# Optimization experiments

Measured on AMD Instinct MI355X. Metric: run time of the kernel, lower is better.

## Reference

```python
import jax, jax.numpy as jnp
import numpy as np

DIM = 128
HEADS = 4
DH = 32
TOPK_RATIO = 0.25
MIN_TOPK = 32
Q_KEEP_RATIO = 0.75
MIN_Q_KEEP = 64
NEG = -1e30


def _layernorm(x, g, b, eps=1e-5):
    mu = x.mean(-1, keepdims=True)
    var = ((x - mu) ** 2).mean(-1, keepdims=True)
    return (x - mu) * jax.lax.rsqrt(var + eps) * g + b


def _topk_scatter_mask(x, k):
    # boolean mask with True at the top-k entries along the last axis (torch scatter_ semantics)
    shp = x.shape
    x2 = x.reshape(-1, shp[-1])
    _, idx = jax.lax.top_k(x2, k)
    rows = jnp.arange(x2.shape[0])[:, None]
    m = jnp.zeros(x2.shape, dtype=bool).at[rows, idx].set(True)
    return m.reshape(shp)


def setup_inputs() -> dict:
    key = jax.random.key(0)
    ks = jax.random.split(key, 24)
    b, n = 1, 6
    x_, y_ = 6, 6
    qw1, qw2 = 16, 16
    kw1, kw2 = 8, 8
    s = 0.02
    inp = {
        'q': jax.random.normal(ks[0], (b, n, x_, y_, qw1, qw2, DIM), jnp.float32),
        'k': jax.random.normal(ks[1], (b, n, x_, y_, kw1, kw2, DIM), jnp.float32),
        'v': jax.random.normal(ks[2], (b, n, x_, y_, kw1, kw2, DIM), jnp.float32),
        'skip': jax.random.normal(ks[3], (b, x_, y_, qw1, qw2, DIM), jnp.float32),
        'logit_bias': jax.random.normal(ks[4], (b, n, 1, 1), jnp.float32),
        'g_q': jnp.ones((DIM,), jnp.float32), 'b_q': jnp.zeros((DIM,), jnp.float32),
        'g_k': jnp.ones((DIM,), jnp.float32), 'b_k': jnp.zeros((DIM,), jnp.float32),
        'g_v': jnp.ones((DIM,), jnp.float32), 'b_v': jnp.zeros((DIM,), jnp.float32),
        'Wq': jax.random.normal(ks[5], (DIM, HEADS * DH), jnp.float32) * s,
        'bq': jnp.zeros((HEADS * DH,), jnp.float32),
        'Wk': jax.random.normal(ks[6], (DIM, HEADS * DH), jnp.float32) * s,
        'bk': jnp.zeros((HEADS * DH,), jnp.float32),
        'Wv': jax.random.normal(ks[7], (DIM, HEADS * DH), jnp.float32) * s,
        'bv': jnp.zeros((HEADS * DH,), jnp.float32),
        'Wp': jax.random.normal(ks[8], (HEADS * DH, DIM), jnp.float32) * s,
        'bp': jnp.zeros((DIM,), jnp.float32),
    }
    return inp


def reference(q, k, v, skip, logit_bias, g_q, b_q, g_k, b_k, g_v, b_v,
              Wq, bq, Wk, bk, Wv, bv, Wp, bp):
    b, n, xh, yw, qw1, qw2, d = q.shape
    _, _, _, _, kw1, kw2, _ = k.shape
    L = xh * yw
    Qn = n * qw1 * qw2
    Kn = n * kw1 * kw2
    H, Dh = HEADS, DH
    scale = Dh ** -0.5

    def win(t, w1, w2, N):
        # b n x y w1 w2 d -> b (x y) (n w1 w2) d
        t = jnp.transpose(t, (0, 2, 3, 1, 4, 5, 6))
        return t.reshape(b, L, N, d)

    qt = win(q, qw1, qw2, Qn)
    kt = win(k, kw1, kw2, Kn)
    vt = win(v, kw1, kw2, Kn)

    qt = _layernorm(qt, g_q, b_q) @ Wq + bq
    kt = _layernorm(kt, g_k, b_k) @ Wk + bk
    vt = _layernorm(vt, g_v, b_v) @ Wv + bv

    def heads(t, N):
        # b l t (h d) -> (b h) l t d
        t = t.reshape(b, L, N, H, Dh)
        t = jnp.transpose(t, (0, 3, 1, 2, 4))
        return t.reshape(b * H, L, N, Dh)

    qh = heads(qt, Qn)
    kh = heads(kt, Kn)
    vh = heads(vt, Kn)

    # dynamic query pruning: keep top-keep_q queries by squared-norm saliency
    keep_q = min(max(max(int(Qn * Q_KEEP_RATIO), MIN_Q_KEEP), 1), Qn)
    sal = jnp.sum(qh * qh, axis=-1)                 # (bh, L, Qn)
    qmask = _topk_scatter_mask(sal, keep_q)
    qh = qh * qmask[..., None]

    logits = jnp.einsum('blqd,blkd->blqk', qh * scale, kh)  # (bh, L, Qn, Kn)

    # OAPE additive logit bias: mean over cameras, tiled (bh index i -> batch i % b)
    lb = logit_bias.mean(axis=1).reshape(b)          # (b,)
    lb_bh = jnp.tile(lb, H)                          # (b*h,) ordering i % b (torch .repeat)
    logits = logits + lb_bh[:, None, None, None]

    topk = max(int(Kn * TOPK_RATIO), MIN_TOPK)
    kmask = _topk_scatter_mask(logits, topk)
    logits = jnp.where(kmask, logits, NEG)
    att = jax.nn.softmax(logits, axis=-1)

    a = jnp.einsum('blqk,blkd->blqd', att, vh)       # (bh, L, Qn, Dh)
    # (b h) l (n w1 w2) d -> b n x y w1 w2 (h d)
    a = a.reshape(b, H, L, n, qw1, qw2, Dh)
    a = jnp.transpose(a, (0, 3, 2, 4, 5, 1, 6)).reshape(b, n, xh, yw, qw1, qw2, H * Dh)

    z = a @ Wp + bp
    z = z.mean(axis=1)                               # mean over cameras
    z = z + skip
    return z
```

## Files before the change

kernel.cpp:

```cpp
#include <hip/hip_runtime.h>
#include <hip/hip_bf16.h>


#define LWIN  36
#define QN    1536
#define KN    384
#define QHS_E 1769472
#define KHS_E 442368
#define KEEPQ 1152

#define SQ_SCALE (0.17677669529663687f * 1.4426950408889634f)

typedef unsigned short ushort_t;
typedef __attribute__((ext_vector_type(8))) short bf16x8;
typedef __attribute__((ext_vector_type(4))) float f32x4;

__device__ __forceinline__ float us2f(unsigned short u) { return __uint_as_float(((unsigned)u) << 16); }
__device__ __forceinline__ unsigned short f2us(float f) { return (unsigned short)(__float_as_uint(f) >> 16); }

__device__ __forceinline__ float fast_exp2(float x) {
#if __has_builtin(__builtin_amdgcn_exp2f)
    return __builtin_amdgcn_exp2f(x);
#else
    return exp2f(x);
#endif
}

__device__ __forceinline__ int wfrag_pos(int k, int n) {
    return ((n >> 4) * 4 + (k >> 5)) * 512 + ((k >> 3) & 3) * 128 + (n & 15) * 8 + (k & 7);
}

__global__ __launch_bounds__(256)
void prep_w_kernel(const float* __restrict__ W0, const float* __restrict__ W1,
                   const float* __restrict__ W2, const float* __restrict__ W3,
                   ushort_t* __restrict__ outw)
{
    const float* W = (blockIdx.x == 0) ? W0 : (blockIdx.x == 1) ? W1
                   : (blockIdx.x == 2) ? W2 : W3;
    const float scl = (blockIdx.x == 0) ? SQ_SCALE : 1.0f;
    __shared__ __align__(16) ushort_t L[16384];
    const int tid = threadIdx.x;
    for (int i = 0; i < 64; ++i) {
        int idx = tid + i * 256;
        int k = idx >> 7, n = idx & 127;
        L[wfrag_pos(k, n)] = f2us(W[idx] * scl);
    }
    __syncthreads();
    uint4* dst = (uint4*)(outw + (size_t)blockIdx.x * 16384);
    const uint4* src = (const uint4*)L;
    for (int i = 0; i < 8; ++i) dst[tid + i * 256] = src[tid + i * 256];
}

__global__ __launch_bounds__(256, 4)
void gemm_proj_kernel(const float* __restrict__ xq, const float* __restrict__ xk,
                      const float* __restrict__ xv,
                      const float* __restrict__ g_q, const float* __restrict__ b_q,
                      const float* __restrict__ g_k, const float* __restrict__ b_k,
                      const float* __restrict__ g_v, const float* __restrict__ b_v,
                      const ushort_t* __restrict__ Wfb,
                      const float* __restrict__ bq, const float* __restrict__ bk,
                      const float* __restrict__ bv,
                      ushort_t* __restrict__ Qh, ushort_t* __restrict__ Kh,
                      ushort_t* __restrict__ Vt, float* __restrict__ sal)
{
    __shared__ __align__(16) ushort_t SB[8704];
    __shared__ __align__(16) float redA[256], redB[256];
    __shared__ float2 mr[64];

    const int b = blockIdx.x;
    const float *xin, *gvec, *bvec, *bias;
    const ushort_t* wf;
    ushort_t* outp;
    float* salp = nullptr;
    int lw2, lw12, ntok, hs_e, mode, t0;
    float bscale = 1.0f;
    if (b < 864) {
        xin = xq; gvec = g_q; bvec = b_q; wf = Wfb; bias = bq; outp = Qh;
        salp = sal; lw2 = 4; lw12 = 8; ntok = QN; hs_e = QHS_E; mode = 0;
        t0 = b * 64; bscale = SQ_SCALE;
    } else if (b < 1080) {
        xin = xk; gvec = g_k; bvec = b_k; wf = Wfb + 16384; bias = bk; outp = Kh;
        lw2 = 3; lw12 = 6; ntok = KN; hs_e = KHS_E; mode = 0; t0 = (b - 864) * 64;
    } else {
        xin = xv; gvec = g_v; bvec = b_v; wf = Wfb + 32768; bias = bv; outp = Vt;
        lw2 = 3; lw12 = 6; ntok = KN; hs_e = 0; mode = 1; t0 = (b - 1080) * 64;
    }

    const int tid = threadIdx.x;

    const int tok = tid >> 2, seg = tid & 3;
    float f[32];
    {
        int t = t0 + tok;
        int l = t / ntok, qn = t - l * ntok;
        int n = qn >> lw12, rr = qn & ((1 << lw12) - 1);
        int a1 = rr >> lw2, a2 = rr & ((1 << lw2) - 1);
        int x = l / 6, y = l - 6 * x;
        size_t off = (size_t)(((((n * 6 + x) * 6 + y) << lw12) + (a1 << lw2) + a2)) * 128;
        const float4* xp = (const float4*)(xin + off) + seg * 8;
        float s = 0.f, s2 = 0.f;
#pragma unroll
        for (int j = 0; j < 8; ++j) {
            float4 v = xp[j];
            f[4 * j + 0] = v.x; f[4 * j + 1] = v.y; f[4 * j + 2] = v.z; f[4 * j + 3] = v.w;
            s += v.x + v.y + v.z + v.w;
            s2 += v.x * v.x + v.y * v.y + v.z * v.z + v.w * v.w;
        }
        redA[tid] = s; redB[tid] = s2;
    }
    __syncthreads();
    if (tid < 64) {
        float4 sa = *(float4*)&redA[tid * 4];
        float4 sb = *(float4*)&redB[tid * 4];
        float s = sa.x + sa.y + sa.z + sa.w;
        float s2 = sb.x + sb.y + sb.z + sb.w;
        float mu = s * (1.0f / 128.0f);
        float var = s2 * (1.0f / 128.0f) - mu * mu;
        mr[tid] = make_float2(mu, rsqrtf(var + 1e-5f));
    }
    __syncthreads();
    {
        float2 m = mr[tok];
#pragma unroll
        for (int qd = 0; qd < 4; ++qd) {
            const float4 g0 = *(const float4*)&gvec[seg * 32 + qd * 8];
            const float4 g1 = *(const float4*)&gvec[seg * 32 + qd * 8 + 4];
            const float4 b0 = *(const float4*)&bvec[seg * 32 + qd * 8];
            const float4 b1 = *(const float4*)&bvec[seg * 32 + qd * 8 + 4];
            float v[8];
            v[0] = (f[qd*8+0] - m.x) * m.y * g0.x + b0.x;
            v[1] = (f[qd*8+1] - m.x) * m.y * g0.y + b0.y;
            v[2] = (f[qd*8+2] - m.x) * m.y * g0.z + b0.z;
            v[3] = (f[qd*8+3] - m.x) * m.y * g0.w + b0.w;
            v[4] = (f[qd*8+4] - m.x) * m.y * g1.x + b1.x;
            v[5] = (f[qd*8+5] - m.x) * m.y * g1.y + b1.y;
            v[6] = (f[qd*8+6] - m.x) * m.y * g1.z + b1.z;
            v[7] = (f[qd*8+7] - m.x) * m.y * g1.w + b1.w;
            uint4 pk;
            pk.x = (unsigned)f2us(v[0]) | ((unsigned)f2us(v[1]) << 16);
            pk.y = (unsigned)f2us(v[2]) | ((unsigned)f2us(v[3]) << 16);
            pk.z = (unsigned)f2us(v[4]) | ((unsigned)f2us(v[5]) << 16);
            pk.w = (unsigned)f2us(v[6]) | ((unsigned)f2us(v[7]) << 16);
            *(uint4*)&SB[((tok >> 4) * 4 + seg) * 512 + qd * 128 + (tok & 15) * 8] = pk;
        }
    }
    __syncthreads();

    const int wv = tid >> 6, lane = tid & 63;
    const int col = lane & 15, quad = lane >> 4;
    f32x4 acc[8];
#pragma unroll
    for (int nt = 0; nt < 8; ++nt) acc[nt] = (f32x4){0.f, 0.f, 0.f, 0.f};
#pragma unroll
    for (int ks = 0; ks < 4; ++ks) {
        bf16x8 a = *(const bf16x8*)&SB[((wv * 4 + ks) * 64 + lane) * 8];
#pragma unroll
        for (int nt = 0; nt < 8; ++nt) {
            bf16x8 bfr = *(const bf16x8*)&wf[((nt * 4 + ks) * 64 + lane) * 8];
            acc[nt] = __builtin_amdgcn_mfma_f32_16x16x32_bf16(a, bfr, acc[nt], 0, 0, 0);
        }
    }
#pragma unroll
    for (int nt = 0; nt < 8; ++nt) {
        float bvv = bias[nt * 16 + col] * bscale;
#pragma unroll
        for (int r = 0; r < 4; ++r) acc[nt][r] += bvv;
    }

    if (salp) {
        float p[4][4];
#pragma unroll
        for (int h = 0; h < 4; ++h)
#pragma unroll
            for (int r = 0; r < 4; ++r)
                p[h][r] = acc[2*h][r] * acc[2*h][r] + acc[2*h+1][r] * acc[2*h+1][r];
#pragma unroll
        for (int sh = 1; sh < 16; sh <<= 1)
#pragma unroll
            for (int h = 0; h < 4; ++h)
#pragma unroll
                for (int r = 0; r < 4; ++r) p[h][r] += __shfl_xor(p[h][r], sh);
        if (col < 4) {
#pragma unroll
            for (int r = 0; r < 4; ++r)
                salp[(size_t)col * (LWIN * ntok) + (t0 + wv * 16 + quad * 4 + r)] = p[col][r];
        }
    }

    __syncthreads();
    if (mode == 0) {
#pragma unroll
        for (int nt = 0; nt < 8; ++nt)
#pragma unroll
            for (int r = 0; r < 4; ++r)
                SB[(nt >> 1) * 2048 + (wv * 16 + quad * 4 + r) * 32 + (nt & 1) * 16 + col] =
                    f2us(acc[nt][r]);
        __syncthreads();
#pragma unroll
        for (int i = 0; i < 4; ++i) {
            int idx16 = tid + i * 256;
            int hh = idx16 >> 8, rem = idx16 & 255;
            *(uint4*)(outp + (size_t)hh * hs_e + (size_t)t0 * 32 + rem * 8) =
                *(const uint4*)&SB[hh * 2048 + rem * 8];
        }
    } else {
#pragma unroll
        for (int nt = 0; nt < 8; ++nt)
#pragma unroll
            for (int r = 0; r < 4; ++r)
                SB[(nt >> 1) * 2176 + ((nt & 1) * 16 + col) * 68 + wv * 16 + quad * 4 + r] =
                    f2us(acc[nt][r]);
        __syncthreads();
        const int l = t0 / KN, kb = t0 - l * KN;
#pragma unroll
        for (int i = 0; i < 2; ++i) {
            int idx16 = tid + i * 256;
            int hh = idx16 >> 7, rem = idx16 & 127;
            int dh = rem >> 2, c = rem & 3;
            *(uint4*)(outp + ((size_t)(hh * LWIN + l) * 32 + dh) * KN + kb + c * 8) =
                *(const uint4*)&SB[hh * 2176 + dh * 68 + c * 8];
        }
    }
}

__global__ __launch_bounds__(64)
void prune_kernel(const float* __restrict__ sal, const ushort_t* __restrict__ Vt,
                  ushort_t* __restrict__ Qh, ushort_t* __restrict__ kidx)
{
    __shared__ __align__(16) ushort_t VmS[32];
    const int lane = threadIdx.x;
    const int h = blockIdx.x / LWIN, l = blockIdx.x % LWIN;

    if (lane < 32) {
        const ushort_t* vrow = Vt + ((size_t)(h * LWIN + l) * 32 + lane) * KN;
        float s = 0.f;
#pragma unroll
        for (int j = 0; j < 96; ++j) s += us2f(vrow[j]);
        VmS[lane] = f2us(s * (1.0f / 96.0f));
    }

    const float* srow = sal + (size_t)h * (LWIN * QN) + (size_t)l * QN;
    unsigned u[24];
#pragma unroll
    for (int i = 0; i < 24; ++i)
        u[i] = __float_as_uint(srow[lane * 24 + i]);

    unsigned lo = 0u, hi = 0x80000000u;
#pragma unroll 1
    while (hi - lo > 1u) {
        unsigned mid = lo + ((hi - lo) >> 1);
        int c = 0;
#pragma unroll
        for (int i = 0; i < 24; ++i) c += (u[i] >= mid);
#pragma unroll
        for (int sh = 32; sh > 0; sh >>= 1) c += __shfl_xor(c, sh);
        if (c >= KEEPQ) lo = mid; else hi = mid;
    }
    const unsigned T = lo;

    int c_gt = 0, eqc = 0;
    int eqpos[24];
#pragma unroll
    for (int i = 0; i < 24; ++i) {
        c_gt += (u[i] > T);
        eqpos[i] = eqc;
        eqc += (u[i] == T);
    }
    int cg = c_gt;
#pragma unroll
    for (int sh = 32; sh > 0; sh >>= 1) cg += __shfl_xor(cg, sh);
    int scanE = eqc;
#pragma unroll
    for (int sh = 1; sh < 64; sh <<= 1) {
        int t = __shfl_up(scanE, sh);
        if (lane >= sh) scanE += t;
    }
    const int preE = scanE - eqc;
    const int need = KEEPQ - cg;

    bool keep[24];
    int kc = 0;
#pragma unroll
    for (int i = 0; i < 24; ++i) {
        keep[i] = (u[i] > T) || ((u[i] == T) && (preE + eqpos[i] < need));
        kc += keep[i];
    }
    int scanK = kc;
#pragma unroll
    for (int sh = 1; sh < 64; sh <<= 1) {
        int t = __shfl_up(scanK, sh);
        if (lane >= sh) scanK += t;
    }
    int posK = scanK - kc;

    __syncthreads();
    const uint4 vm0 = *(const uint4*)&VmS[0];
    const uint4 vm1 = *(const uint4*)&VmS[8];
    const uint4 vm2 = *(const uint4*)&VmS[16];
    const uint4 vm3 = *(const uint4*)&VmS[24];

    ushort_t* kout  = kidx + (size_t)(h * LWIN + l) * KEEPQ;
    ushort_t* qbase = Qh + (size_t)h * QHS_E + (size_t)l * QN * 32;
#pragma unroll 1
    for (int i = 0; i < 24; ++i) {
        if (keep[i]) {
            kout[posK++] = (ushort_t)(lane * 24 + i);
        } else {
            uint4* p = (uint4*)(qbase + (size_t)(lane * 24 + i) * 32);
            p[0] = vm0; p[1] = vm1; p[2] = vm2; p[3] = vm3;
        }
    }
}

__global__ __launch_bounds__(256, 3)
void attn_kernel(ushort_t* __restrict__ Qh, const ushort_t* __restrict__ Kh,
                 const ushort_t* __restrict__ Vt, const ushort_t* __restrict__ kidx)
{
    __shared__ __align__(16) ushort_t Ks[KN * 36];
    __shared__ __align__(16) ushort_t Vs[32 * 390];

    const int tid = threadIdx.x;
    const int qt = blockIdx.x, l = blockIdx.y, h = blockIdx.z;

    const ushort_t* kg = Kh + (size_t)h * KHS_E + (size_t)l * (KN * 32);
#pragma unroll
    for (int i = 0; i < 12; ++i) {
        int idx = tid + i * 256;
        int key = idx >> 3, c = idx & 7;
        *(uint2*)&Ks[key * 36 + c * 4] = *(const uint2*)&kg[idx * 4];
    }
    const ushort_t* vg = Vt + (size_t)(h * LWIN + l) * (32 * KN);
#pragma unroll
    for (int i = 0; i < 12; ++i) {
        int idx = tid + i * 256;
        int dh = idx / 96, c = idx - dh * 96;
        *(uint2*)&Vs[dh * 390 + c * 4] = *(const uint2*)&vg[idx * 4];
    }

    const int lane = tid & 63, wv = tid >> 6;
    const int col = lane & 15, quad = lane >> 4;

    const ushort_t* kr = kidx + (size_t)(h * LWIN + l) * KEEPQ + qt * 64 + wv * 16;
    const int rowA = kr[col];
    const ushort_t* qhl = Qh + (size_t)h * QHS_E + (size_t)l * QN * 32;
    const bf16x8 aq = *(const bf16x8*)(qhl + (size_t)rowA * 32 + quad * 8);
    __syncthreads();

    f32x4 s[24];
#pragma unroll
    for (int t = 0; t < 24; ++t) s[t] = (f32x4){0.f, 0.f, 0.f, 0.f};
#pragma unroll
    for (int t = 0; t < 24; ++t) {
        bf16x8 bk = *(const bf16x8*)&Ks[(16 * t + col) * 36 + quad * 8];
        s[t] = __builtin_amdgcn_mfma_f32_16x16x32_bf16(aq, bk, s[t], 0, 0, 0);
    }
    __syncthreads();

    float vmax[4], vmin[4];
#pragma unroll
    for (int r = 0; r < 4; ++r) { vmax[r] = s[0][r]; vmin[r] = s[0][r]; }
#pragma unroll
    for (int t = 1; t < 24; ++t)
#pragma unroll
        for (int r = 0; r < 4; ++r) {
            vmax[r] = fmaxf(vmax[r], s[t][r]);
            vmin[r] = fminf(vmin[r], s[t][r]);
        }
#pragma unroll
    for (int sh = 1; sh < 16; sh <<= 1)
#pragma unroll
        for (int r = 0; r < 4; ++r) {
            vmax[r] = fmaxf(vmax[r], __shfl_xor(vmax[r], sh));
            vmin[r] = fminf(vmin[r], __shfl_xor(vmin[r], sh));
        }

    float lo[4], hi[4];
#pragma unroll
    for (int r = 0; r < 4; ++r) { lo[r] = vmin[r] - 1.0f; hi[r] = vmax[r]; }
    for (int it = 0; it < 10; ++it) {
        float mid[4]; int cnt[4];
#pragma unroll
        for (int r = 0; r < 4; ++r) { mid[r] = 0.5f * (lo[r] + hi[r]); cnt[r] = 0; }
#pragma unroll
        for (int t = 0; t < 24; ++t)
#pragma unroll
            for (int r = 0; r < 4; ++r) cnt[r] += (s[t][r] > mid[r]);
#pragma unroll
        for (int sh = 1; sh < 16; sh <<= 1)
#pragma unroll
            for (int r = 0; r < 4; ++r) cnt[r] += __shfl_xor(cnt[r], sh);
#pragma unroll
        for (int r = 0; r < 4; ++r) {
            if (cnt[r] >= 96) lo[r] = mid[r]; else hi[r] = mid[r];
        }
    }

    float sum[4];
#pragma unroll
    for (int r = 0; r < 4; ++r) sum[r] = 0.f;
#pragma unroll
    for (int t = 0; t < 24; ++t)
#pragma unroll
        for (int r = 0; r < 4; ++r) {
            float e = (s[t][r] > lo[r]) ? fast_exp2(s[t][r] - vmax[r]) : 0.f;
            s[t][r] = e; sum[r] += e;
        }
#pragma unroll
    for (int sh = 1; sh < 16; sh <<= 1)
#pragma unroll
        for (int r = 0; r < 4; ++r) sum[r] += __shfl_xor(sum[r], sh);
    float inv[4];
#pragma unroll
    for (int r = 0; r < 4; ++r) inv[r] = 1.0f / sum[r];

    f32x4 o0 = (f32x4){0.f, 0.f, 0.f, 0.f};
    f32x4 o1 = (f32x4){0.f, 0.f, 0.f, 0.f};
    ushort_t* pb = Ks + wv * 1088;
#pragma unroll
    for (int ch = 0; ch < 6; ++ch) {
#pragma unroll
        for (int tl = 0; tl < 4; ++tl) {
            int t = 4 * ch + tl;
#pragma unroll
            for (int r = 0; r < 4; ++r)
                pb[(quad * 4 + r) * 68 + 16 * tl + col] = f2us(s[t][r]);
        }
#pragma unroll
        for (int ks = 0; ks < 2; ++ks) {
            bf16x8 ap  = *(const bf16x8*)&pb[col * 68 + ks * 32 + quad * 8];
            bf16x8 bv0 = *(const bf16x8*)&Vs[col * 390 + ch * 64 + ks * 32 + quad * 8];
            bf16x8 bv1 = *(const bf16x8*)&Vs[(16 + col) * 390 + ch * 64 + ks * 32 + quad * 8];
            o0 = __builtin_amdgcn_mfma_f32_16x16x32_bf16(ap, bv0, o0, 0, 0, 0);
            o1 = __builtin_amdgcn_mfma_f32_16x16x32_bf16(ap, bv1, o1, 0, 0, 0);
        }
    }

#pragma unroll
    for (int r = 0; r < 4; ++r) {
        ushort_t* oq = (ushort_t*)qhl + (size_t)kr[quad * 4 + r] * 32;
        oq[col]      = f2us(o0[r] * inv[r]);
        oq[16 + col] = f2us(o1[r] * inv[r]);
    }
}

__global__ __launch_bounds__(256, 4)
void gemm_out_kernel(const ushort_t* __restrict__ aS,
                     const ushort_t* __restrict__ Wfrag,
                     const float* __restrict__ bp,
                     const float* __restrict__ skip,
                     float* __restrict__ outp)
{
    __shared__ __align__(16) ushort_t SB[8192];

    const int tid = threadIdx.x;
    const int t0 = blockIdx.x * 64;

    const int tok = tid >> 2, h = tid & 3;
    {
        int t = t0 + tok;
        int l = t >> 8, qq = t & 255;
        float f[32];
#pragma unroll
        for (int e = 0; e < 32; ++e) f[e] = 0.f;
#pragma unroll
        for (int n = 0; n < 6; ++n) {
            const ushort_t* p = aS + (size_t)h * QHS_E + ((size_t)l * QN + n * 256 + qq) * 32;
#pragma unroll
            for (int c = 0; c < 4; ++c) {
                ushort4 va = *(const ushort4*)(p + c * 8);
                ushort4 vb = *(const ushort4*)(p + c * 8 + 4);
                f[c*8+0] += us2f(va.x); f[c*8+1] += us2f(va.y);
                f[c*8+2] += us2f(va.z); f[c*8+3] += us2f(va.w);
                f[c*8+4] += us2f(vb.x); f[c*8+5] += us2f(vb.y);
                f[c*8+6] += us2f(vb.z); f[c*8+7] += us2f(vb.w);
            }
        }
#pragma unroll
        for (int qd = 0; qd < 4; ++qd) {
            uint4 pk;
            pk.x = (unsigned)f2us(f[qd*8+0] * (1.f/6.f)) | ((unsigned)f2us(f[qd*8+1] * (1.f/6.f)) << 16);
            pk.y = (unsigned)f2us(f[qd*8+2] * (1.f/6.f)) | ((unsigned)f2us(f[qd*8+3] * (1.f/6.f)) << 16);
            pk.z = (unsigned)f2us(f[qd*8+4] * (1.f/6.f)) | ((unsigned)f2us(f[qd*8+5] * (1.f/6.f)) << 16);
            pk.w = (unsigned)f2us(f[qd*8+6] * (1.f/6.f)) | ((unsigned)f2us(f[qd*8+7] * (1.f/6.f)) << 16);
            *(uint4*)&SB[((tok >> 4) * 4 + h) * 512 + qd * 128 + (tok & 15) * 8] = pk;
        }
    }
    __syncthreads();

    const int wv = tid >> 6, lane = tid & 63;
    const int col = lane & 15, quad = lane >> 4;
    f32x4 acc[8];
#pragma unroll
    for (int nt = 0; nt < 8; ++nt) acc[nt] = (f32x4){0.f, 0.f, 0.f, 0.f};
#pragma unroll
    for (int ks = 0; ks < 4; ++ks) {
        bf16x8 a = *(const bf16x8*)&SB[((wv * 4 + ks) * 64 + lane) * 8];
#pragma unroll
        for (int nt = 0; nt < 8; ++nt) {
            bf16x8 bfr = *(const bf16x8*)&Wfrag[((nt * 4 + ks) * 64 + lane) * 8];
            acc[nt] = __builtin_amdgcn_mfma_f32_16x16x32_bf16(a, bfr, acc[nt], 0, 0, 0);
        }
    }
#pragma unroll
    for (int nt = 0; nt < 8; ++nt) {
        float bv = bp[nt * 16 + col];
#pragma unroll
        for (int r = 0; r < 4; ++r) {
            int trow = t0 + wv * 16 + quad * 4 + r;
            size_t gi = (size_t)trow * 128 + nt * 16 + col;
            outp[gi] = acc[nt][r] + bv + skip[gi];
        }
    }
}

extern "C" void kernel_launch(void* const* d_in, const int* in_sizes, int n_in,
                              void* d_out, int out_size, void* d_ws, size_t ws_size,
                              hipStream_t stream)
{
    (void)in_sizes; (void)n_in; (void)out_size; (void)ws_size;
    const float* q    = (const float*)d_in[0];
    const float* k    = (const float*)d_in[1];
    const float* v    = (const float*)d_in[2];
    const float* skip = (const float*)d_in[3];
    const float* g_q = (const float*)d_in[5];
    const float* b_q = (const float*)d_in[6];
    const float* g_k = (const float*)d_in[7];
    const float* b_k = (const float*)d_in[8];
    const float* g_v = (const float*)d_in[9];
    const float* b_v = (const float*)d_in[10];
    const float* Wq  = (const float*)d_in[11];
    const float* bq  = (const float*)d_in[12];
    const float* Wk  = (const float*)d_in[13];
    const float* bk  = (const float*)d_in[14];
    const float* Wv  = (const float*)d_in[15];
    const float* bv  = (const float*)d_in[16];
    const float* Wp  = (const float*)d_in[17];
    const float* bp  = (const float*)d_in[18];

    ushort_t* Qh = (ushort_t*)d_ws;
    ushort_t* Kh = Qh + (size_t)4 * QHS_E;
    ushort_t* Vt = Kh + (size_t)4 * KHS_E;
    float*   sal = (float*)(Vt + (size_t)4 * KHS_E);
    ushort_t* Wf = (ushort_t*)(sal + (size_t)4 * LWIN * QN);
    ushort_t* kidx = Wf + (size_t)4 * 16384;

    prep_w_kernel<<<4, 256, 0, stream>>>(Wq, Wk, Wv, Wp, Wf);
    gemm_proj_kernel<<<1296, 256, 0, stream>>>(q, k, v, g_q, b_q, g_k, b_k, g_v, b_v,
                                               Wf, bq, bk, bv, Qh, Kh, Vt, sal);
    prune_kernel<<<144, 64, 0, stream>>>(sal, Vt, Qh, kidx);
    attn_kernel<<<dim3(18, LWIN, 4), 256, 0, stream>>>(Qh, Kh, Vt, kidx);
    gemm_out_kernel<<<144, 256, 0, stream>>>(Qh, Wf + 3 * 16384, bp, skip, (float*)d_out);
}
```

Before: 269.0 us.

## Split small kernels across more blocks and narrow top-k bisection range

```diff
diff --git a/kernel.cpp b/kernel.cpp
--- a/kernel.cpp
+++ b/kernel.cpp
@@ -35,20 +35,21 @@
                    const float* __restrict__ W2, const float* __restrict__ W3,
                    ushort_t* __restrict__ outw)
 {
-    const float* W = (blockIdx.x == 0) ? W0 : (blockIdx.x == 1) ? W1
-                   : (blockIdx.x == 2) ? W2 : W3;
-    const float scl = (blockIdx.x == 0) ? SQ_SCALE : 1.0f;
-    __shared__ __align__(16) ushort_t L[16384];
+    const int m = blockIdx.x >> 1, half = blockIdx.x & 1;
+    const float* W = (m == 0) ? W0 : (m == 1) ? W1 : (m == 2) ? W2 : W3;
+    const float scl = (m == 0) ? SQ_SCALE : 1.0f;
+    __shared__ __align__(16) ushort_t L[8192];
     const int tid = threadIdx.x;
-    for (int i = 0; i < 64; ++i) {
+    const int nbase = half * 64;
+    for (int i = 0; i < 32; ++i) {
         int idx = tid + i * 256;
-        int k = idx >> 7, n = idx & 127;
-        L[wfrag_pos(k, n)] = f2us(W[idx] * scl);
-    }
-    __syncthreads();
-    uint4* dst = (uint4*)(outw + (size_t)blockIdx.x * 16384);
+        int k = idx >> 6, n0 = idx & 63;
+        L[wfrag_pos(k, nbase + n0) - half * 8192] = f2us(W[k * 128 + nbase + n0] * scl);
+    }
+    __syncthreads();
+    uint4* dst = (uint4*)(outw + (size_t)m * 16384 + half * 8192);
     const uint4* src = (const uint4*)L;
-    for (int i = 0; i < 8; ++i) dst[tid + i * 256] = src[tid + i * 256];
+    for (int i = 0; i < 4; ++i) dst[tid + i * 256] = src[tid + i * 256];
 }
 
 __global__ __launch_bounds__(256, 4)
@@ -231,12 +232,18 @@
     const int lane = threadIdx.x;
     const int h = blockIdx.x / LWIN, l = blockIdx.x % LWIN;
 
-    if (lane < 32) {
-        const ushort_t* vrow = Vt + ((size_t)(h * LWIN + l) * 32 + lane) * KN;
+    {
+        const int dh = lane >> 1, hf = lane & 1;
+        const ushort_t* vrow = Vt + ((size_t)(h * LWIN + l) * 32 + dh) * KN + hf * 48;
         float s = 0.f;
 #pragma unroll
-        for (int j = 0; j < 96; ++j) s += us2f(vrow[j]);
-        VmS[lane] = f2us(s * (1.0f / 96.0f));
+        for (int j = 0; j < 12; ++j) {
+            uint2 u = *(const uint2*)&vrow[j * 4];
+            s += us2f((ushort_t)(u.x & 0xffff)) + us2f((ushort_t)(u.x >> 16))
+               + us2f((ushort_t)(u.y & 0xffff)) + us2f((ushort_t)(u.y >> 16));
+        }
+        s += __shfl_xor(s, 1);
+        if (hf == 0) VmS[dh] = f2us(s * (1.0f / 96.0f));
     }
 
     const float* srow = sal + (size_t)h * (LWIN * QN) + (size_t)l * QN;
@@ -356,28 +363,22 @@
     }
     __syncthreads();
 
-    float vmax[4], vmin[4];
-#pragma unroll
-    for (int r = 0; r < 4; ++r) { vmax[r] = s[0][r]; vmin[r] = s[0][r]; }
+    float vmax[4];
+#pragma unroll
+    for (int r = 0; r < 4; ++r) vmax[r] = s[0][r];
 #pragma unroll
     for (int t = 1; t < 24; ++t)
 #pragma unroll
-        for (int r = 0; r < 4; ++r) {
-            vmax[r] = fmaxf(vmax[r], s[t][r]);
-            vmin[r] = fminf(vmin[r], s[t][r]);
-        }
+        for (int r = 0; r < 4; ++r) vmax[r] = fmaxf(vmax[r], s[t][r]);
 #pragma unroll
     for (int sh = 1; sh < 16; sh <<= 1)
 #pragma unroll
-        for (int r = 0; r < 4; ++r) {
-            vmax[r] = fmaxf(vmax[r], __shfl_xor(vmax[r], sh));
-            vmin[r] = fminf(vmin[r], __shfl_xor(vmin[r], sh));
-        }
+        for (int r = 0; r < 4; ++r) vmax[r] = fmaxf(vmax[r], __shfl_xor(vmax[r], sh));
 
     float lo[4], hi[4];
 #pragma unroll
-    for (int r = 0; r < 4; ++r) { lo[r] = vmin[r] - 1.0f; hi[r] = vmax[r]; }
-    for (int it = 0; it < 10; ++it) {
+    for (int r = 0; r < 4; ++r) { lo[r] = vmax[r] - 32.0f; hi[r] = vmax[r]; }
+    for (int it = 0; it < 8; ++it) {
         float mid[4]; int cnt[4];
 #pragma unroll
         for (int r = 0; r < 4; ++r) { mid[r] = 0.5f * (lo[r] + hi[r]); cnt[r] = 0; }
@@ -443,17 +444,17 @@
     }
 }
 
-__global__ __launch_bounds__(256, 4)
+__global__ __launch_bounds__(128)
 void gemm_out_kernel(const ushort_t* __restrict__ aS,
                      const ushort_t* __restrict__ Wfrag,
                      const float* __restrict__ bp,
                      const float* __restrict__ skip,
                      float* __restrict__ outp)
 {
-    __shared__ __align__(16) ushort_t SB[8192];
+    __shared__ __align__(16) ushort_t SB[4096];
 
     const int tid = threadIdx.x;
-    const int t0 = blockIdx.x * 64;
+    const int t0 = blockIdx.x * 32;
 
     const int tok = tid >> 2, h = tid & 3;
     {
@@ -544,10 +545,10 @@
     ushort_t* Wf = (ushort_t*)(sal + (size_t)4 * LWIN * QN);
     ushort_t* kidx = Wf + (size_t)4 * 16384;
 
-    prep_w_kernel<<<4, 256, 0, stream>>>(Wq, Wk, Wv, Wp, Wf);
+    prep_w_kernel<<<8, 256, 0, stream>>>(Wq, Wk, Wv, Wp, Wf);
     gemm_proj_kernel<<<1296, 256, 0, stream>>>(q, k, v, g_q, b_q, g_k, b_k, g_v, b_v,
                                                Wf, bq, bk, bv, Qh, Kh, Vt, sal);
     prune_kernel<<<144, 64, 0, stream>>>(sal, Vt, Qh, kidx);
     attn_kernel<<<dim3(18, LWIN, 4), 256, 0, stream>>>(Qh, Kh, Vt, kidx);
-    gemm_out_kernel<<<144, 256, 0, stream>>>(Qh, Wf + 3 * 16384, bp, skip, (float*)d_out);
-}
+    gemm_out_kernel<<<288, 128, 0, stream>>>(Qh, Wf + 3 * 16384, bp, skip, (float*)d_out);
+}
```

After: 252.3 us. 6.2% less time.
